# Kernel optimization log

Hardware: AMD Instinct MI355X
Metric: run time of the kernel (lower is better)

Reference implementation:

```python
import jax, jax.numpy as jnp
import numpy as np

EPS = 1.1920929e-07  # torch.finfo(float32).eps
TOP_K = 2
AUX_COEF = 0.01

def rmsnorm(x):
    return x * jax.lax.rsqrt(jnp.mean(x * x, axis=-1, keepdims=True) + EPS)

def setup_inputs() -> dict:
    key = jax.random.key(0)
    ks = jax.random.split(key, 8)
    B, T, C, H, E = 1, 2048, 1024, 2048, 8
    x = jax.random.normal(ks[0], (B, T, C), jnp.float32)
    gate_w = jax.random.normal(ks[1], (E, C), jnp.float32) * 0.02
    w1 = jax.random.normal(ks[2], (E, H, C), jnp.float32) * 0.02  # expert up-proj
    w2 = jax.random.normal(ks[3], (E, C, H), jnp.float32) * 0.02  # expert down-proj
    shared_gate_w = jax.random.normal(ks[4], (1, C), jnp.float32) * 0.02
    k_w = jax.random.normal(ks[5], (H, C), jnp.float32) * 0.02
    k_b = jax.random.normal(ks[6], (H,), jnp.float32) * 0.01
    v_w = jax.random.normal(ks[7], (C, H), jnp.float32) * 0.02
    v_b = jnp.zeros((C,), jnp.float32)
    return dict(x=x, gate_w=gate_w, w1=w1, w2=w2, shared_gate_w=shared_gate_w,
                k_w=k_w, k_b=k_b, v_w=v_w, v_b=v_b)

def reference(x, gate_w, w1, w2, shared_gate_w, k_w, k_b, v_w, v_b):
    B, T, C = x.shape
    xt = rmsnorm(x.reshape(-1, C))                     # [N,C]
    N = xt.shape[0]
    raw = xt @ gate_w.T                                # [N,E]
    scores = jax.nn.softmax(raw, axis=-1)
    topk_w, topk_idx = jax.lax.top_k(scores, TOP_K)    # [N,k]
    topk_w = topk_w / (jnp.sum(topk_w, axis=-1, keepdims=True) + 1e-6)
    E = scores.shape[-1]
    rows = jnp.arange(N)[:, None]
    onehot = jnp.zeros_like(scores).at[rows, topk_idx].set(1.0 / TOP_K)
    aux_loss = E * jnp.sum(jnp.mean(onehot, 0) * jnp.mean(scores, 0)) * AUX_COEF
    # dense gate matrix [N,E]: combine weight per (token, expert)
    g = jnp.zeros_like(scores).at[rows, topk_idx].add(topk_w)
    # grouped-GEMM expressed densely over experts (reference math identical)
    h = jnp.einsum('nc,ehc->neh', xt, w1)              # [N,E,H]
    h = jnp.square(jax.nn.relu(h)) * g[:, :, None]     # act + gate-combine weight
    out = jnp.einsum('neh,ech->nc', h, w2)             # [N,C]
    # shared expert: sigmoid gate * MLP (MLP re-norms its input)
    sg = jax.nn.sigmoid(xt @ shared_gate_w.T)          # [N,1]
    xs = rmsnorm(xt)
    kk = jnp.square(jax.nn.relu(xs @ k_w.T + k_b))     # [N,H]
    shared = kk @ v_w.T + v_b                          # [N,C]
    out = out + sg * shared
    return out.reshape(B, T, C), aux_loss
```

## Files before the change

### kernel.cpp

```cpp
#include <hip/hip_runtime.h>
#include <hip/hip_bf16.h>
#include <stdint.h>

typedef __bf16 bf16;
typedef bf16 bf16x8 __attribute__((ext_vector_type(8)));
typedef bf16 bf16x4 __attribute__((ext_vector_type(4)));
typedef float f32x4 __attribute__((ext_vector_type(4)));

constexpr int N = 2048;
constexpr int C = 1024;
constexpr int H = 2048;
constexpr int E = 8;
constexpr float EPS = 1.1920929e-07f;

constexpr int BM = 128, BN = 128;
constexpr int GT = 32;
constexpr int SUB = 8192;

constexpr int PREP_GATE = N / GT;
constexpr int PREP_RMS  = N;
constexpr int CVT1_F4   = (E * H * C + H * C) / 4;
constexpr int CVT1_BLK  = CVT1_F4 / 1024;
constexpr int PREP_TOTAL = PREP_GATE + PREP_RMS + CVT1_BLK;

constexpr int P1_UP    = (H / BN) * (N / BM) * E;
constexpr int P1_KP    = (N / BM) * (H / BN);
constexpr int CVT2_F4  = (E * C * H + C * H) / 4;
constexpr int CVT2_BLK = CVT2_F4 / 1024;
constexpr int P1_TOTAL = P1_UP + P1_KP + CVT2_BLK;

constexpr int P2_DOWN  = (C / BN) * (N / BM) * (E * 2);
constexpr int P2_VP    = (N / BM) * (C / BN) * 2;
constexpr int P2_TOTAL = P2_DOWN + P2_VP;

constexpr int COMBINE_BLK = (N * C / 4) / 256;

__device__ __forceinline__ void cvt_pair(const float* __restrict__ s1, bf16* __restrict__ d1,
                                         size_t n1, const float* __restrict__ s2,
                                         bf16* __restrict__ d2, int cbx) {
  size_t base = (size_t)cbx * 1024 + threadIdx.x;
  #pragma unroll
  for (int j = 0; j < 4; ++j) {
    size_t i = base + (size_t)j * 256;
    if (i < n1) {
      float4 v = ((const float4*)s1)[i];
      bf16x4 o = { (bf16)v.x, (bf16)v.y, (bf16)v.z, (bf16)v.w };
      ((bf16x4*)d1)[i] = o;
    } else {
      size_t k = i - n1;
      float4 v = ((const float4*)s2)[k];
      bf16x4 o = { (bf16)v.x, (bf16)v.y, (bf16)v.z, (bf16)v.w };
      ((bf16x4*)d2)[k] = o;
    }
  }
}

__global__ __launch_bounds__(256) void prep_kernel(
    const float* __restrict__ x, const float* __restrict__ gate_w,
    const float* __restrict__ sgw, const float* __restrict__ w1,
    const float* __restrict__ kw,
    bf16* __restrict__ xtb, float* __restrict__ rs2_arr,
    float* __restrict__ g, float* __restrict__ sgbuf,
    int* __restrict__ counts, int* __restrict__ lists,
    float* __restrict__ scoresums,
    bf16* __restrict__ w1b, bf16* __restrict__ kwb) {
  __shared__ float wsm[9][1024];
  __shared__ float s_scores[8];
  __shared__ int   s_cnt[8];
  __shared__ int   s_base[8];
  __shared__ int   s_e1[GT], s_p1[GT], s_e2[GT], s_p2[GT];
  const int bx = blockIdx.x;
  const int tid = threadIdx.x, lane = tid & 63, wave = tid >> 6;

  if (bx >= PREP_GATE + PREP_RMS) {
    cvt_pair(w1, w1b, (size_t)E * H * C / 4, kw, kwb, bx - PREP_GATE - PREP_RMS);
    return;
  }
  if (bx >= PREP_GATE) {
    int n = bx - PREP_GATE;
    float4 v = ((const float4*)(x + (size_t)n * C))[tid];
    float ss = v.x*v.x + v.y*v.y + v.z*v.z + v.w*v.w;
    #pragma unroll
    for (int off = 32; off > 0; off >>= 1) ss += __shfl_down(ss, off, 64);
    __shared__ float red[4];
    __shared__ float tot;
    if (lane == 0) red[wave] = ss;
    __syncthreads();
    if (tid == 0) tot = red[0] + red[1] + red[2] + red[3];
    __syncthreads();
    float sumsq = tot;
    float rs1 = rsqrtf(sumsq * (1.f / C) + EPS);
    bf16x4 o = { (bf16)(v.x*rs1), (bf16)(v.y*rs1), (bf16)(v.z*rs1), (bf16)(v.w*rs1) };
    ((bf16x4*)(xtb + (size_t)n * C))[tid] = o;
    if (tid == 0) {
      float m2 = sumsq * rs1 * rs1 * (1.f / C);
      rs2_arr[n] = rsqrtf(m2 + EPS);
    }
    return;
  }
  for (int i = tid; i < 9 * 1024; i += 256) {
    int e = i >> 10, c = i & 1023;
    wsm[e][c] = (e < 8) ? gate_w[i] : sgw[c];
  }
  if (tid < 8) { s_scores[tid] = 0.f; s_cnt[tid] = 0; }
  __syncthreads();

  const int tok0 = bx * GT + wave * (GT / 4);
  for (int tt = 0; tt < GT / 4; ++tt) {
    const int tok = tok0 + tt;
    const float* xr = x + (size_t)tok * C;
    float acc[10];
    #pragma unroll
    for (int e = 0; e < 10; e++) acc[e] = 0.f;
    #pragma unroll
    for (int k = 0; k < 16; ++k) {
      int c = k * 64 + lane;
      float xv = xr[c];
      #pragma unroll
      for (int e = 0; e < 9; e++) acc[e] = fmaf(xv, wsm[e][c], acc[e]);
      acc[9] = fmaf(xv, xv, acc[9]);
    }
    #pragma unroll
    for (int e = 0; e < 10; e++) {
      float v = acc[e];
      #pragma unroll
      for (int off = 32; off > 0; off >>= 1) v += __shfl_xor(v, off, 64);
      acc[e] = v;
    }
    if (lane == 0) {
      float rs1 = rsqrtf(acc[9] * (1.f / C) + EPS);
      float raw[9];
      #pragma unroll
      for (int e = 0; e < 9; e++) raw[e] = acc[e] * rs1;
      float m = raw[0];
      for (int e = 1; e < 8; e++) m = fmaxf(m, raw[e]);
      float sc[8], s = 0.f;
      for (int e = 0; e < 8; e++) { sc[e] = expf(raw[e] - m); s += sc[e]; }
      float inv = 1.f / s;
      for (int e = 0; e < 8; e++) sc[e] *= inv;
      int i1 = 0;
      for (int e = 1; e < 8; e++) if (sc[e] > sc[i1]) i1 = e;
      int i2 = -1;
      for (int e = 0; e < 8; e++) {
        if (e == i1) continue;
        if (i2 < 0 || sc[e] > sc[i2]) i2 = e;
      }
      float denom = sc[i1] + sc[i2] + 1e-6f;
      float* gr = g + (size_t)tok * E;
      #pragma unroll
      for (int e = 0; e < 8; e++) gr[e] = 0.f;
      gr[i1] = sc[i1] / denom;
      gr[i2] = sc[i2] / denom;
      sgbuf[tok] = 1.f / (1.f + expf(-raw[8]));
      for (int e = 0; e < 8; e++) atomicAdd(&s_scores[e], sc[e]);
      int lt = wave * (GT / 4) + tt;
      int p1 = atomicAdd(&s_cnt[i1], 1);
      int p2 = atomicAdd(&s_cnt[i2], 1);
      s_e1[lt] = i1; s_p1[lt] = p1;
      s_e2[lt] = i2; s_p2[lt] = p2;
    }
  }
  __syncthreads();
  if (tid < 8) {
    s_base[tid] = atomicAdd(&counts[tid], s_cnt[tid]);
    atomicAdd(&scoresums[tid], s_scores[tid]);
  }
  __syncthreads();
  if (tid < GT) {
    int tok = bx * GT + tid;
    int e1 = s_e1[tid], e2 = s_e2[tid];
    lists[e1 * N + s_base[e1] + s_p1[tid]] = (tok << 1);
    lists[e2 * N + s_base[e2] + s_p2[tid]] = (tok << 1) | 1;
  }
}

#define GLL(gp, lp)                                                             \
  __builtin_amdgcn_global_load_lds((__attribute__((address_space(1))) void*)(gp), \
                                   (__attribute__((address_space(3))) void*)(lp), 16, 0, 0)

__device__ __forceinline__ void mfma_loop(
    const char* gA0, const char* gA1, const char* gB0, const char* gB1,
    char* As, char* Bs, int wave, int lane, int kIters64,
    int mb, int nb, f32x4 acc[4][4]) {
  const int l0 = wave * 2048, l1 = l0 + 1024;
  const int arow = lane & 15;
  const int koff = (lane >> 4) * 16;
  for (int kt = 0; kt < kIters64; ++kt) {
    GLL(gA0,      As + l0);        GLL(gA1,      As + l1);
    GLL(gB0,      Bs + l0);        GLL(gB1,      Bs + l1);
    GLL(gA0 + 64, As + SUB + l0);  GLL(gA1 + 64, As + SUB + l1);
    GLL(gB0 + 64, Bs + SUB + l0);  GLL(gB1 + 64, Bs + SUB + l1);
    gA0 += 128; gA1 += 128; gB0 += 128; gB1 += 128;
    __syncthreads();
    #pragma unroll
    for (int kh = 0; kh < 2; ++kh) {
      const char* Ac = As + kh * SUB;
      const char* Bc = Bs + kh * SUB;
      bf16x8 a[4], b[4];
      #pragma unroll
      for (int i = 0; i < 4; ++i) {
        a[i] = *(const bf16x8*)(Ac + (mb + i * 16 + arow) * 64 + koff);
        b[i] = *(const bf16x8*)(Bc + (nb + i * 16 + arow) * 64 + koff);
      }
      #pragma unroll
      for (int i = 0; i < 4; ++i)
        #pragma unroll
        for (int j = 0; j < 4; ++j)
          acc[i][j] = __builtin_amdgcn_mfma_f32_16x16x32_bf16(a[i], b[j], acc[i][j], 0, 0, 0);
    }
    __syncthreads();
  }
}

#define GEMM_VARS                                                  \
  const int tid = threadIdx.x;                                     \
  const int lane = tid & 63, wave = tid >> 6;                      \
  const int sr0 = wave * 32 + (lane >> 2), sr1 = sr0 + 16;         \
  const int scb = (lane & 3) * 16;          \
  const int mb = (wave & 1) * 64, nb = (wave >> 1) * 64;           \
  const int col = lane & 15, quad = lane >> 4;                     \
  f32x4 acc[4][4] = {};

__device__ __forceinline__ void run_up(
    const bf16* __restrict__ xtb, const bf16* __restrict__ w1b,
    const float* __restrict__ g, const int* __restrict__ lists,
    const int* __restrict__ counts, bf16* __restrict__ hb,
    int e, int m0, int h0, char* As, char* Bs, int* toks) {
  const int cnt = counts[e];
  if (m0 >= cnt) return;
  GEMM_VARS
  if (tid < BM) toks[tid] = lists[e * N + min(m0 + tid, cnt - 1)];
  __syncthreads();
  const char* gA0 = (const char*)xtb + ((size_t)(toks[sr0] >> 1) * C) * 2 + scb;
  const char* gA1 = (const char*)xtb + ((size_t)(toks[sr1] >> 1) * C) * 2 + scb;
  const char* gB0 = (const char*)w1b + ((size_t)e * H * C + (size_t)(h0 + sr0) * C) * 2 + scb;
  const char* gB1 = (const char*)w1b + ((size_t)e * H * C + (size_t)(h0 + sr1) * C) * 2 + scb;
  mfma_loop(gA0, gA1, gB0, gB1, As, Bs, wave, lane, C / 64, mb, nb, acc);
  #pragma unroll
  for (int mi = 0; mi < 4; mi++) {
    #pragma unroll
    for (int r = 0; r < 4; r++) {
      int ml = mb + mi * 16 + quad * 4 + r;
      if (m0 + ml < cnt) {
        int packed = toks[ml];
        float gv = g[(size_t)(packed >> 1) * E + e];
        size_t base = (size_t)packed * H + h0 + nb;
        #pragma unroll
        for (int ni = 0; ni < 4; ni++) {
          float v = fmaxf(acc[mi][ni][r], 0.f);
          hb[base + ni * 16 + col] = (bf16)(v * v * gv);
        }
      }
    }
  }
}

__device__ __forceinline__ void run_kproj(
    const bf16* __restrict__ xtb, const bf16* __restrict__ kwb,
    const float* __restrict__ rs2, const float* __restrict__ k_b,
    bf16* __restrict__ kkb, int n0, int h0, char* As, char* Bs) {
  GEMM_VARS
  const char* gA0 = (const char*)xtb + ((size_t)(n0 + sr0) * C) * 2 + scb;
  const char* gA1 = (const char*)xtb + ((size_t)(n0 + sr1) * C) * 2 + scb;
  const char* gB0 = (const char*)kwb + ((size_t)(h0 + sr0) * C) * 2 + scb;
  const char* gB1 = (const char*)kwb + ((size_t)(h0 + sr1) * C) * 2 + scb;
  mfma_loop(gA0, gA1, gB0, gB1, As, Bs, wave, lane, C / 64, mb, nb, acc);
  #pragma unroll
  for (int mi = 0; mi < 4; mi++) {
    #pragma unroll
    for (int r = 0; r < 4; r++) {
      int n = n0 + mb + mi * 16 + quad * 4 + r;
      float rs = rs2[n];
      #pragma unroll
      for (int ni = 0; ni < 4; ni++) {
        int h = h0 + nb + ni * 16 + col;
        float v = fmaf(acc[mi][ni][r], rs, k_b[h]);
        v = fmaxf(v, 0.f);
        kkb[(size_t)n * H + h] = (bf16)(v * v);
      }
    }
  }
}

__device__ __forceinline__ void run_down(
    const bf16* __restrict__ hb, const bf16* __restrict__ w2b,
    const int* __restrict__ lists, const int* __restrict__ counts,
    float* __restrict__ dp, int e, int ks, int m0, int c0,
    char* As, char* Bs, int* toks) {
  const int cnt = counts[e];
  if (m0 >= cnt) return;
  GEMM_VARS
  if (tid < BM) toks[tid] = lists[e * N + min(m0 + tid, cnt - 1)];
  __syncthreads();
  const size_t kofs = (size_t)ks * (H / 2) * 2;
  const char* gA0 = (const char*)hb + ((size_t)toks[sr0] * H) * 2 + kofs + scb;
  const char* gA1 = (const char*)hb + ((size_t)toks[sr1] * H) * 2 + kofs + scb;
  const char* gB0 = (const char*)w2b + ((size_t)e * C * H + (size_t)(c0 + sr0) * H) * 2 + kofs + scb;
  const char* gB1 = (const char*)w2b + ((size_t)e * C * H + (size_t)(c0 + sr1) * H) * 2 + kofs + scb;
  mfma_loop(gA0, gA1, gB0, gB1, As, Bs, wave, lane, (H / 2) / 64, mb, nb, acc);
  #pragma unroll
  for (int mi = 0; mi < 4; mi++) {
    #pragma unroll
    for (int r = 0; r < 4; r++) {
      int ml = mb + mi * 16 + quad * 4 + r;
      if (m0 + ml < cnt) {
        int packed = toks[ml];
        int tok = packed >> 1, par = packed & 1;
        float* orow = dp + (((size_t)(ks * 2 + par) * N + tok) * C) + c0 + nb;
        #pragma unroll
        for (int ni = 0; ni < 4; ni++) orow[ni * 16 + col] = acc[mi][ni][r];
      }
    }
  }
}

__device__ __forceinline__ void run_vproj(
    const bf16* __restrict__ kkb, const bf16* __restrict__ vwb,
    float* __restrict__ vp, int n0, int c0, int ks, char* As, char* Bs) {
  GEMM_VARS
  const size_t kofs = (size_t)ks * (H / 2) * 2;
  const char* gA0 = (const char*)kkb + ((size_t)(n0 + sr0) * H) * 2 + kofs + scb;
  const char* gA1 = (const char*)kkb + ((size_t)(n0 + sr1) * H) * 2 + kofs + scb;
  const char* gB0 = (const char*)vwb + ((size_t)(c0 + sr0) * H) * 2 + kofs + scb;
  const char* gB1 = (const char*)vwb + ((size_t)(c0 + sr1) * H) * 2 + kofs + scb;
  mfma_loop(gA0, gA1, gB0, gB1, As, Bs, wave, lane, (H / 2) / 64, mb, nb, acc);
  #pragma unroll
  for (int mi = 0; mi < 4; mi++) {
    #pragma unroll
    for (int r = 0; r < 4; r++) {
      int n = n0 + mb + mi * 16 + quad * 4 + r;
      float* orow = vp + ((size_t)ks * N + n) * C + c0 + nb;
      #pragma unroll
      for (int ni = 0; ni < 4; ni++) orow[ni * 16 + col] = acc[mi][ni][r];
    }
  }
}

__global__ __launch_bounds__(256) void phase1_kernel(
    const bf16* __restrict__ xtb, const bf16* __restrict__ w1b,
    const float* __restrict__ g, const int* __restrict__ lists,
    const int* __restrict__ counts, bf16* __restrict__ hb,
    const bf16* __restrict__ kwb, const float* __restrict__ rs2,
    const float* __restrict__ k_b, bf16* __restrict__ kkb,
    const float* __restrict__ w2, const float* __restrict__ vw,
    bf16* __restrict__ w2b, bf16* __restrict__ vwb) {
  __shared__ __align__(16) char As[2 * SUB];
  __shared__ __align__(16) char Bs[2 * SUB];
  __shared__ int toks[BM];
  const int bx = blockIdx.x;
  if (bx < P1_UP) {
    int e = bx >> 8, rem = bx & 255;
    int h0 = (rem & 15) * BN, m0 = (rem >> 4) * BM;
    run_up(xtb, w1b, g, lists, counts, hb, e, m0, h0, As, Bs, toks);
  } else if (bx < P1_UP + P1_KP) {
    int rem = bx - P1_UP;
    int n0 = (rem & 15) * BM, h0 = (rem >> 4) * BN;
    run_kproj(xtb, kwb, rs2, k_b, kkb, n0, h0, As, Bs);
  } else {
    cvt_pair(w2, w2b, (size_t)E * C * H / 4, vw, vwb, bx - P1_UP - P1_KP);
  }
}

__global__ __launch_bounds__(256) void phase2_kernel(
    const bf16* __restrict__ hb, const bf16* __restrict__ w2b,
    const int* __restrict__ lists, const int* __restrict__ counts,
    const bf16* __restrict__ kkb, const bf16* __restrict__ vwb,
    float* __restrict__ dp, float* __restrict__ vp) {
  __shared__ __align__(16) char As[2 * SUB];
  __shared__ __align__(16) char Bs[2 * SUB];
  __shared__ int toks[BM];
  const int bx = blockIdx.x;
  if (bx < P2_DOWN) {
    int z = bx >> 7, rem = bx & 127;
    int e = z >> 1, ks = z & 1;
    int c0 = (rem & 7) * BN, m0 = (rem >> 3) * BM;
    run_down(hb, w2b, lists, counts, dp, e, ks, m0, c0, As, Bs, toks);
  } else {
    int rem = bx - P2_DOWN;
    int ks = rem >> 7, r2 = rem & 127;
    int n0 = (r2 & 15) * BM, c0 = (r2 >> 4) * BN;
    run_vproj(kkb, vwb, vp, n0, c0, ks, As, Bs);
  }
}

__global__ __launch_bounds__(256) void combine_kernel(
    const float* __restrict__ dp, const float* __restrict__ vp,
    const float* __restrict__ v_b, const float* __restrict__ sg,
    float* __restrict__ out) {
  constexpr size_t NC = (size_t)N * C;
  size_t i = (size_t)blockIdx.x * 256 + threadIdx.x;
  size_t off = i * 4;
  int n = (int)(off >> 10);
  int c = (int)(off & 1023);
  float4 a = ((const float4*)(dp))[i];
  float4 b = ((const float4*)(dp + NC))[i];
  float4 d2 = ((const float4*)(dp + 2 * NC))[i];
  float4 d3 = ((const float4*)(dp + 3 * NC))[i];
  float4 u = ((const float4*)(vp))[i];
  float4 w = ((const float4*)(vp + NC))[i];
  float4 bias = *(const float4*)(v_b + c);
  float s = sg[n];
  float4 o;
  o.x = a.x + b.x + d2.x + d3.x + s * (u.x + w.x + bias.x);
  o.y = a.y + b.y + d2.y + d3.y + s * (u.y + w.y + bias.y);
  o.z = a.z + b.z + d2.z + d3.z + s * (u.z + w.z + bias.z);
  o.w = a.w + b.w + d2.w + d3.w + s * (u.w + w.w + bias.w);
  ((float4*)out)[i] = o;
}

__global__ void aux_kernel(const float* __restrict__ scoresums,
                           const int* __restrict__ counts,
                           float* __restrict__ out_aux) {
  if (threadIdx.x == 0) {
    float a = 0.f;
    for (int e = 0; e < 8; e++)
      a += (0.5f * (float)counts[e] * (1.f / N)) * (scoresums[e] * (1.f / N));
    out_aux[0] = 8.f * a * 0.01f;
  }
}

extern "C" void kernel_launch(void* const* d_in, const int* in_sizes, int n_in,
                              void* d_out, int out_size, void* d_ws, size_t ws_size,
                              hipStream_t stream) {
  (void)in_sizes; (void)n_in; (void)ws_size;
  const float* x   = (const float*)d_in[0];
  const float* gw  = (const float*)d_in[1];
  const float* w1  = (const float*)d_in[2];
  const float* w2  = (const float*)d_in[3];
  const float* sgw = (const float*)d_in[4];
  const float* k_w = (const float*)d_in[5];
  const float* k_b = (const float*)d_in[6];
  const float* v_w = (const float*)d_in[7];
  const float* v_b = (const float*)d_in[8];
  float* out = (float*)d_out;

  char* p = (char*)d_ws;
  auto alloc = [&](size_t bytes) { char* r = p; p += (bytes + 255) & ~255ull; return r; };
  bf16* xtb  = (bf16*)alloc((size_t)N * C * 2);
  bf16* w1b  = (bf16*)alloc((size_t)E * H * C * 2);
  bf16* w2b  = (bf16*)alloc((size_t)E * C * H * 2);
  bf16* kwb  = (bf16*)alloc((size_t)H * C * 2);
  bf16* vwb  = (bf16*)alloc((size_t)C * H * 2);
  bf16* hb   = (bf16*)alloc((size_t)2 * N * H * 2);
  bf16* kkb  = (bf16*)alloc((size_t)N * H * 2);
  float* rs2 = (float*)alloc((size_t)N * 4);
  float* g   = (float*)alloc((size_t)N * E * 4);
  float* sg  = (float*)alloc((size_t)N * 4);
  float* scoresums = (float*)alloc(256);
  int* counts = (int*)alloc(256);
  int* lists  = (int*)alloc((size_t)E * N * 4);
  float* vp   = (float*)alloc((size_t)2 * N * C * 4);
  float* dp   = (float*)w1b;

  hipMemsetAsync(d_out, 0, (size_t)out_size * sizeof(float), stream);
  hipMemsetAsync(scoresums, 0, 512, stream);
  prep_kernel<<<PREP_TOTAL, 256, 0, stream>>>(
      x, gw, sgw, w1, k_w, xtb, rs2, g, sg, counts, lists, scoresums, w1b, kwb);
  phase1_kernel<<<P1_TOTAL, 256, 0, stream>>>(
      xtb, w1b, g, lists, counts, hb, kwb, rs2, k_b, kkb, w2, v_w, w2b, vwb);
  phase2_kernel<<<P2_TOTAL, 256, 0, stream>>>(
      hb, w2b, lists, counts, kkb, vwb, dp, vp);
  combine_kernel<<<COMBINE_BLK, 256, 0, stream>>>(dp, vp, v_b, sg, out);
  aux_kernel<<<1, 64, 0, stream>>>(scoresums, counts, out + (size_t)N * C);
}
```

Measured before the change: 295.3 us.

## Widen GEMM tiles to 128x256 with 512-thread blocks and move w2 conversion to prep

The GEMM tile grows from 128x128 to 128x256, and blocks grow to 8 waves, each still computing a 64x64 sub-tile. This means each A tile loaded into LDS is reused across twice as many output columns, which cuts global and LDS traffic per FLOP. The fp32-to-bf16 conversion of w2 and v_w moves out of phase1 into prep_kernel, so phase1 only runs GEMMs. The costs are larger LDS use per block, fewer blocks (which may underfill the CUs), and more serialized conversion work in prep.

```diff
diff --git a/kernel.cpp b/kernel.cpp
--- a/kernel.cpp
+++ b/kernel.cpp
@@ -13,23 +13,21 @@
 constexpr int E = 8;
 constexpr float EPS = 1.1920929e-07f;
 
-constexpr int BM = 128, BN = 128;
+constexpr int BM = 128, BN = 256;
 constexpr int GT = 32;
-constexpr int SUB = 8192;
+constexpr int ASUB = 128 * 64;
+constexpr int BSUB = 256 * 64;
 
 constexpr int PREP_GATE = N / GT;
 constexpr int PREP_RMS  = N;
-constexpr int CVT1_F4   = (E * H * C + H * C) / 4;
-constexpr int CVT1_BLK  = CVT1_F4 / 1024;
-constexpr int PREP_TOTAL = PREP_GATE + PREP_RMS + CVT1_BLK;
-
-constexpr int P1_UP    = (H / BN) * (N / BM) * E;
+constexpr int CVT_BLK   = ((E * H * C + H * C) / 4) / 1024;
+constexpr int PREP_TOTAL = PREP_GATE + PREP_RMS + 2 * CVT_BLK;
+
+constexpr int P1_UP    = E * (N / BM) * (H / BN);
 constexpr int P1_KP    = (N / BM) * (H / BN);
-constexpr int CVT2_F4  = (E * C * H + C * H) / 4;
-constexpr int CVT2_BLK = CVT2_F4 / 1024;
-constexpr int P1_TOTAL = P1_UP + P1_KP + CVT2_BLK;
-
-constexpr int P2_DOWN  = (C / BN) * (N / BM) * (E * 2);
+constexpr int P1_TOTAL = P1_UP + P1_KP;
+
+constexpr int P2_DOWN  = (E * 2) * (N / BM) * (C / BN);
 constexpr int P2_VP    = (N / BM) * (C / BN) * 2;
 constexpr int P2_TOTAL = P2_DOWN + P2_VP;
 
@@ -58,12 +56,14 @@
 __global__ __launch_bounds__(256) void prep_kernel(
     const float* __restrict__ x, const float* __restrict__ gate_w,
     const float* __restrict__ sgw, const float* __restrict__ w1,
-    const float* __restrict__ kw,
+    const float* __restrict__ kw, const float* __restrict__ w2,
+    const float* __restrict__ vw,
     bf16* __restrict__ xtb, float* __restrict__ rs2_arr,
     float* __restrict__ g, float* __restrict__ sgbuf,
     int* __restrict__ counts, int* __restrict__ lists,
     float* __restrict__ scoresums,
-    bf16* __restrict__ w1b, bf16* __restrict__ kwb) {
+    bf16* __restrict__ w1b, bf16* __restrict__ kwb,
+    bf16* __restrict__ w2b, bf16* __restrict__ vwb) {
   __shared__ float wsm[9][1024];
   __shared__ float s_scores[8];
   __shared__ int   s_cnt[8];
@@ -72,6 +72,11 @@
   const int bx = blockIdx.x;
   const int tid = threadIdx.x, lane = tid & 63, wave = tid >> 6;
 
+  if (bx >= PREP_GATE + PREP_RMS + CVT_BLK) {
+    cvt_pair(w2, w2b, (size_t)E * C * H / 4, vw, vwb,
+             bx - PREP_GATE - PREP_RMS - CVT_BLK);
+    return;
+  }
   if (bx >= PREP_GATE + PREP_RMS) {
     cvt_pair(w1, w1b, (size_t)E * H * C / 4, kw, kwb, bx - PREP_GATE - PREP_RMS);
     return;
@@ -179,23 +184,21 @@
                                    (__attribute__((address_space(3))) void*)(lp), 16, 0, 0)
 
 __device__ __forceinline__ void mfma_loop(
-    const char* gA0, const char* gA1, const char* gB0, const char* gB1,
-    char* As, char* Bs, int wave, int lane, int kIters64,
-    int mb, int nb, f32x4 acc[4][4]) {
-  const int l0 = wave * 2048, l1 = l0 + 1024;
+    const char* pA, const char* pB0, const char* pB1,
+    char* As, char* Bs, int dA, int dB0, int dB1,
+    int lane, int kIters, int mb, int nb, f32x4 acc[4][4]) {
   const int arow = lane & 15;
   const int koff = (lane >> 4) * 16;
-  for (int kt = 0; kt < kIters64; ++kt) {
-    GLL(gA0,      As + l0);        GLL(gA1,      As + l1);
-    GLL(gB0,      Bs + l0);        GLL(gB1,      Bs + l1);
-    GLL(gA0 + 64, As + SUB + l0);  GLL(gA1 + 64, As + SUB + l1);
-    GLL(gB0 + 64, Bs + SUB + l0);  GLL(gB1 + 64, Bs + SUB + l1);
-    gA0 += 128; gA1 += 128; gB0 += 128; gB1 += 128;
+  for (int kt = 0; kt < kIters; ++kt) {
+    GLL(pA,       As + dA);          GLL(pA  + 64, As + ASUB + dA);
+    GLL(pB0,      Bs + dB0);         GLL(pB0 + 64, Bs + BSUB + dB0);
+    GLL(pB1,      Bs + dB1);         GLL(pB1 + 64, Bs + BSUB + dB1);
+    pA += 128; pB0 += 128; pB1 += 128;
     __syncthreads();
     #pragma unroll
     for (int kh = 0; kh < 2; ++kh) {
-      const char* Ac = As + kh * SUB;
-      const char* Bc = Bs + kh * SUB;
+      const char* Ac = As + kh * ASUB;
+      const char* Bc = Bs + kh * BSUB;
       bf16x8 a[4], b[4];
       #pragma unroll
       for (int i = 0; i < 4; ++i) {
@@ -214,10 +217,13 @@
 
 #define GEMM_VARS                                                  \
   const int tid = threadIdx.x;                                     \
-  const int lane = tid & 63, wave = tid >> 6;                      \
-  const int sr0 = wave * 32 + (lane >> 2), sr1 = sr0 + 16;         \
-  const int scb = (lane & 3) * 16;          \
-  const int mb = (wave & 1) * 64, nb = (wave >> 1) * 64;           \
+  const int lane = tid & 63, wave = tid >> 6;            \
+  const int mb = (wave >> 2) * 64, nb = (wave & 3) * 64;           \
+  const int srow = wave * 16 + (lane >> 2);       \
+  const int scb = (lane & 3) * 16;              \
+  const int dA  = wave * 1024;                      \
+  const int dB0 = wave * 1024;                                     \
+  const int dB1 = 8192 + wave * 1024;                              \
   const int col = lane & 15, quad = lane >> 4;                     \
   f32x4 acc[4][4] = {};
 
@@ -231,11 +237,10 @@
   GEMM_VARS
   if (tid < BM) toks[tid] = lists[e * N + min(m0 + tid, cnt - 1)];
   __syncthreads();
-  const char* gA0 = (const char*)xtb + ((size_t)(toks[sr0] >> 1) * C) * 2 + scb;
-  const char* gA1 = (const char*)xtb + ((size_t)(toks[sr1] >> 1) * C) * 2 + scb;
-  const char* gB0 = (const char*)w1b + ((size_t)e * H * C + (size_t)(h0 + sr0) * C) * 2 + scb;
-  const char* gB1 = (const char*)w1b + ((size_t)e * H * C + (size_t)(h0 + sr1) * C) * 2 + scb;
-  mfma_loop(gA0, gA1, gB0, gB1, As, Bs, wave, lane, C / 64, mb, nb, acc);
+  const char* pA  = (const char*)xtb + ((size_t)(toks[srow] >> 1) * C) * 2 + scb;
+  const char* pB0 = (const char*)w1b + ((size_t)e * H * C + (size_t)(h0 + srow) * C) * 2 + scb;
+  const char* pB1 = (const char*)w1b + ((size_t)e * H * C + (size_t)(h0 + 128 + srow) * C) * 2 + scb;
+  mfma_loop(pA, pB0, pB1, As, Bs, dA, dB0, dB1, lane, C / 64, mb, nb, acc);
   #pragma unroll
   for (int mi = 0; mi < 4; mi++) {
     #pragma unroll
@@ -260,11 +265,10 @@
     const float* __restrict__ rs2, const float* __restrict__ k_b,
     bf16* __restrict__ kkb, int n0, int h0, char* As, char* Bs) {
   GEMM_VARS
-  const char* gA0 = (const char*)xtb + ((size_t)(n0 + sr0) * C) * 2 + scb;
-  const char* gA1 = (const char*)xtb + ((size_t)(n0 + sr1) * C) * 2 + scb;
-  const char* gB0 = (const char*)kwb + ((size_t)(h0 + sr0) * C) * 2 + scb;
-  const char* gB1 = (const char*)kwb + ((size_t)(h0 + sr1) * C) * 2 + scb;
-  mfma_loop(gA0, gA1, gB0, gB1, As, Bs, wave, lane, C / 64, mb, nb, acc);
+  const char* pA  = (const char*)xtb + ((size_t)(n0 + srow) * C) * 2 + scb;
+  const char* pB0 = (const char*)kwb + ((size_t)(h0 + srow) * C) * 2 + scb;
+  const char* pB1 = (const char*)kwb + ((size_t)(h0 + 128 + srow) * C) * 2 + scb;
+  mfma_loop(pA, pB0, pB1, As, Bs, dA, dB0, dB1, lane, C / 64, mb, nb, acc);
   #pragma unroll
   for (int mi = 0; mi < 4; mi++) {
     #pragma unroll
@@ -293,11 +297,10 @@
   if (tid < BM) toks[tid] = lists[e * N + min(m0 + tid, cnt - 1)];
   __syncthreads();
   const size_t kofs = (size_t)ks * (H / 2) * 2;
-  const char* gA0 = (const char*)hb + ((size_t)toks[sr0] * H) * 2 + kofs + scb;
-  const char* gA1 = (const char*)hb + ((size_t)toks[sr1] * H) * 2 + kofs + scb;
-  const char* gB0 = (const char*)w2b + ((size_t)e * C * H + (size_t)(c0 + sr0) * H) * 2 + kofs + scb;
-  const char* gB1 = (const char*)w2b + ((size_t)e * C * H + (size_t)(c0 + sr1) * H) * 2 + kofs + scb;
-  mfma_loop(gA0, gA1, gB0, gB1, As, Bs, wave, lane, (H / 2) / 64, mb, nb, acc);
+  const char* pA  = (const char*)hb + ((size_t)toks[srow] * H) * 2 + kofs + scb;
+  const char* pB0 = (const char*)w2b + ((size_t)e * C * H + (size_t)(c0 + srow) * H) * 2 + kofs + scb;
+  const char* pB1 = (const char*)w2b + ((size_t)e * C * H + (size_t)(c0 + 128 + srow) * H) * 2 + kofs + scb;
+  mfma_loop(pA, pB0, pB1, As, Bs, dA, dB0, dB1, lane, (H / 2) / 64, mb, nb, acc);
   #pragma unroll
   for (int mi = 0; mi < 4; mi++) {
     #pragma unroll
@@ -319,11 +322,10 @@
     float* __restrict__ vp, int n0, int c0, int ks, char* As, char* Bs) {
   GEMM_VARS
   const size_t kofs = (size_t)ks * (H / 2) * 2;
-  const char* gA0 = (const char*)kkb + ((size_t)(n0 + sr0) * H) * 2 + kofs + scb;
-  const char* gA1 = (const char*)kkb + ((size_t)(n0 + sr1) * H) * 2 + kofs + scb;
-  const char* gB0 = (const char*)vwb + ((size_t)(c0 + sr0) * H) * 2 + kofs + scb;
-  const char* gB1 = (const char*)vwb + ((size_t)(c0 + sr1) * H) * 2 + kofs + scb;
-  mfma_loop(gA0, gA1, gB0, gB1, As, Bs, wave, lane, (H / 2) / 64, mb, nb, acc);
+  const char* pA  = (const char*)kkb + ((size_t)(n0 + srow) * H) * 2 + kofs + scb;
+  const char* pB0 = (const char*)vwb + ((size_t)(c0 + srow) * H) * 2 + kofs + scb;
+  const char* pB1 = (const char*)vwb + ((size_t)(c0 + 128 + srow) * H) * 2 + kofs + scb;
+  mfma_loop(pA, pB0, pB1, As, Bs, dA, dB0, dB1, lane, (H / 2) / 64, mb, nb, acc);
   #pragma unroll
   for (int mi = 0; mi < 4; mi++) {
     #pragma unroll
@@ -336,48 +338,44 @@
   }
 }
 
-__global__ __launch_bounds__(256) void phase1_kernel(
+__global__ __launch_bounds__(512) void phase1_kernel(
     const bf16* __restrict__ xtb, const bf16* __restrict__ w1b,
     const float* __restrict__ g, const int* __restrict__ lists,
     const int* __restrict__ counts, bf16* __restrict__ hb,
     const bf16* __restrict__ kwb, const float* __restrict__ rs2,
-    const float* __restrict__ k_b, bf16* __restrict__ kkb,
-    const float* __restrict__ w2, const float* __restrict__ vw,
-    bf16* __restrict__ w2b, bf16* __restrict__ vwb) {
-  __shared__ __align__(16) char As[2 * SUB];
-  __shared__ __align__(16) char Bs[2 * SUB];
+    const float* __restrict__ k_b, bf16* __restrict__ kkb) {
+  __shared__ __align__(16) char As[2 * ASUB];
+  __shared__ __align__(16) char Bs[2 * BSUB];
   __shared__ int toks[BM];
   const int bx = blockIdx.x;
   if (bx < P1_UP) {
-    int e = bx >> 8, rem = bx & 255;
-    int h0 = (rem & 15) * BN, m0 = (rem >> 4) * BM;
+    int e = bx >> 7, rem = bx & 127;
+    int h0 = (rem & 7) * BN, m0 = (rem >> 3) * BM;
     run_up(xtb, w1b, g, lists, counts, hb, e, m0, h0, As, Bs, toks);
-  } else if (bx < P1_UP + P1_KP) {
+  } else {
     int rem = bx - P1_UP;
     int n0 = (rem & 15) * BM, h0 = (rem >> 4) * BN;
     run_kproj(xtb, kwb, rs2, k_b, kkb, n0, h0, As, Bs);
-  } else {
-    cvt_pair(w2, w2b, (size_t)E * C * H / 4, vw, vwb, bx - P1_UP - P1_KP);
-  }
-}
-
-__global__ __launch_bounds__(256) void phase2_kernel(
+  }
+}
+
+__global__ __launch_bounds__(512) void phase2_kernel(
     const bf16* __restrict__ hb, const bf16* __restrict__ w2b,
     const int* __restrict__ lists, const int* __restrict__ counts,
     const bf16* __restrict__ kkb, const bf16* __restrict__ vwb,
     float* __restrict__ dp, float* __restrict__ vp) {
-  __shared__ __align__(16) char As[2 * SUB];
-  __shared__ __align__(16) char Bs[2 * SUB];
+  __shared__ __align__(16) char As[2 * ASUB];
+  __shared__ __align__(16) char Bs[2 * BSUB];
   __shared__ int toks[BM];
   const int bx = blockIdx.x;
   if (bx < P2_DOWN) {
-    int z = bx >> 7, rem = bx & 127;
+    int z = bx >> 6, rem = bx & 63;
     int e = z >> 1, ks = z & 1;
-    int c0 = (rem & 7) * BN, m0 = (rem >> 3) * BM;
+    int c0 = (rem & 3) * BN, m0 = (rem >> 2) * BM;
     run_down(hb, w2b, lists, counts, dp, e, ks, m0, c0, As, Bs, toks);
   } else {
     int rem = bx - P2_DOWN;
-    int ks = rem >> 7, r2 = rem & 127;
+    int ks = rem >> 6, r2 = rem & 63;
     int n0 = (r2 & 15) * BM, c0 = (r2 >> 4) * BN;
     run_vproj(kkb, vwb, vp, n0, c0, ks, As, Bs);
   }
@@ -455,10 +453,11 @@
   hipMemsetAsync(d_out, 0, (size_t)out_size * sizeof(float), stream);
   hipMemsetAsync(scoresums, 0, 512, stream);
   prep_kernel<<<PREP_TOTAL, 256, 0, stream>>>(
-      x, gw, sgw, w1, k_w, xtb, rs2, g, sg, counts, lists, scoresums, w1b, kwb);
-  phase1_kernel<<<P1_TOTAL, 256, 0, stream>>>(
-      xtb, w1b, g, lists, counts, hb, kwb, rs2, k_b, kkb, w2, v_w, w2b, vwb);
-  phase2_kernel<<<P2_TOTAL, 256, 0, stream>>>(
+      x, gw, sgw, w1, k_w, w2, v_w, xtb, rs2, g, sg, counts, lists, scoresums,
+      w1b, kwb, w2b, vwb);
+  phase1_kernel<<<P1_TOTAL, 512, 0, stream>>>(
+      xtb, w1b, g, lists, counts, hb, kwb, rs2, k_b, kkb);
+  phase2_kernel<<<P2_TOTAL, 512, 0, stream>>>(
       hb, w2b, lists, counts, kkb, vwb, dp, vp);
   combine_kernel<<<COMBINE_BLK, 256, 0, stream>>>(dp, vp, v_b, sg, out);
   aux_kernel<<<1, 64, 0, stream>>>(scoresums, counts, out + (size_t)N * C);
```

Result: no change. 295.0 us (-0.1%).
